# Performance work log

Hardware: AMD Instinct MI355X
Metric: run time of the kernel (lower is better)

The kernel has to match this reference:

```python
import jax, jax.numpy as jnp
import numpy as np

B, S, D, H, DH = 2, 2048, 768, 12, 64
GAMMA = 0.5
SMOOTHING = 1.0  # softmax_attn_smoothing scalar (non-trainable weight in the original)
SCALE = 1.0 / float(np.sqrt(DH))


def setup_inputs() -> dict:
    key = jax.random.key(0)
    ks = jax.random.split(key, 8)
    w = 0.02
    return {
        "inp": jax.random.normal(ks[0], (B, S, D), dtype=jnp.float32),
        "pos_emb": jax.random.normal(ks[1], (S, D), dtype=jnp.float32),
        "Wq_inp": jax.random.normal(ks[2], (D, H * DH), dtype=jnp.float32) * w,
        "Wk_inp": jax.random.normal(ks[3], (D, H * DH), dtype=jnp.float32) * w,
        "Wq_pos": jax.random.normal(ks[4], (D, H * DH), dtype=jnp.float32) * w,
        "Wk_pos": jax.random.normal(ks[5], (D, H * DH), dtype=jnp.float32) * w,
        "Wv": jax.random.normal(ks[6], (D, H * DH), dtype=jnp.float32) * w,
        "Wo": jax.random.normal(ks[7], (H * DH, D), dtype=jnp.float32) * w,
    }


def reference(inp, pos_emb, Wq_inp, Wk_inp, Wq_pos, Wk_pos, Wv, Wo):
    # projections; note original reshape order: [..., d_head, n_head]
    q_i = (inp @ Wq_inp).reshape(B, S, DH, H)
    k_i = (inp @ Wk_inp).reshape(B, S, DH, H)
    q_p = (pos_emb @ Wq_pos).reshape(S, DH, H)
    k_p = (pos_emb @ Wk_pos).reshape(S, DH, H)
    v = (inp @ Wv).reshape(B, S, DH, H)

    # content-content stream: [B,S,S,H], softmax over key axis (axis=2)
    score_inp = jnp.einsum("bidh,bjdh->bijh", q_i, k_i) * (SCALE * SMOOTHING)
    prob_inp = jax.nn.softmax(score_inp, axis=2)

    # position-position stream: [S,S,H], softmax over key axis (axis=1)
    score_pos = jnp.einsum("idh,jdh->ijh", q_p, k_p) * (SCALE * SMOOTHING)
    prob_pos = jax.nn.softmax(score_pos, axis=1)[None]  # [1,S,S,H]

    # gamma blend of the two attention distributions
    attn_prob = (1.0 - GAMMA) * prob_inp + GAMMA * prob_pos  # [B,S,S,H]

    # V-weighted sum, merge heads as [..., h, d] per the original 'bihd' output
    attn_out = jnp.einsum("bijh,bjdh->bihd", attn_prob, v).reshape(B, S, H * DH)
    attn_out = attn_out @ Wo  # [B,S,D]
    return attn_out, attn_prob
```

## Files before the change

kernel.cpp:

```cpp
#include <hip/hip_runtime.h>
#include <hip/hip_bf16.h>

constexpr int NH  = 12;
constexpr int SEQ = 2048;
constexpr int DHD = 64;
constexpr int DIM = 768;

typedef __bf16 bf16x8 __attribute__((ext_vector_type(8)));
typedef __bf16 bf16x4 __attribute__((ext_vector_type(4)));
typedef float  f32x4  __attribute__((ext_vector_type(4)));

#define MFMA16(a, b, c) __builtin_amdgcn_mfma_f32_16x16x32_bf16((a), (b), (c), 0, 0, 0)

__global__ __launch_bounds__(256) void proj_kernel(
    const float* __restrict__ inp, const float* __restrict__ pos,
    const float* __restrict__ Wqi, const float* __restrict__ Wki,
    const float* __restrict__ Wqp, const float* __restrict__ Wkp,
    const float* __restrict__ Wvv,
    __bf16* __restrict__ Qi, __bf16* __restrict__ Ki, __bf16* __restrict__ Vt,
    __bf16* __restrict__ Qp, __bf16* __restrict__ Kp)
{
    const int z = blockIdx.z;
    const float* A; const float* W; __bf16* outp; int M; int mode; float scale = 1.0f;
    if (z == 0)      { A = inp; W = Wqi; outp = Qi; M = 4096; mode = 0; scale = 0.125f; }
    else if (z == 1) { A = inp; W = Wki; outp = Ki; M = 4096; mode = 0; }
    else if (z == 2) { A = inp; W = Wvv; outp = Vt; M = 4096; mode = 1; }
    else if (z == 3) { A = pos; W = Wqp; outp = Qp; M = 2048; mode = 2; scale = 0.125f; }
    else             { A = pos; W = Wkp; outp = Kp; M = 2048; mode = 2; }

    const int m0 = blockIdx.y * 64;
    if (m0 >= M) return;
    const int n0 = blockIdx.x * 192;

    __shared__ __bf16 Al[64][32];
    __shared__ __bf16 Wl[192][32];

    const int tid = threadIdx.x;
    const int lane = tid & 63, wv = tid >> 6;
    const int wm = wv >> 1, wn = wv & 1;
    const int l15 = lane & 15, lg = lane >> 4;

    f32x4 c[2][6] = {};

    for (int kt = 0; kt < 24; ++kt) {
        const int k0 = kt * 32;
        __syncthreads();
        {
            const int r = tid >> 3, kq = tid & 7;
            #pragma unroll
            for (int rep = 0; rep < 2; ++rep) {
                const float4 v = *reinterpret_cast<const float4*>(
                    &A[(size_t)(m0 + r + rep * 32) * DIM + k0 + kq * 4]);
                bf16x4 t;
                t[0] = (__bf16)v.x; t[1] = (__bf16)v.y; t[2] = (__bf16)v.z; t[3] = (__bf16)v.w;
                *reinterpret_cast<bf16x4*>(&Al[r + rep * 32][kq * 4]) = t;
            }
        }
        for (int idx = tid; idx < 32 * 48; idx += 256) {
            const int k = idx / 48, nq = idx - k * 48;
            const float4 v = *reinterpret_cast<const float4*>(
                &W[(size_t)(k0 + k) * DIM + n0 + nq * 4]);
            Wl[nq * 4 + 0][k] = (__bf16)v.x;
            Wl[nq * 4 + 1][k] = (__bf16)v.y;
            Wl[nq * 4 + 2][k] = (__bf16)v.z;
            Wl[nq * 4 + 3][k] = (__bf16)v.w;
        }
        __syncthreads();

        bf16x8 a[2], b[6];
        #pragma unroll
        for (int mf = 0; mf < 2; ++mf)
            a[mf] = *reinterpret_cast<const bf16x8*>(&Al[wm * 32 + mf * 16 + l15][lg * 8]);
        #pragma unroll
        for (int nf = 0; nf < 6; ++nf)
            b[nf] = *reinterpret_cast<const bf16x8*>(&Wl[wn * 96 + nf * 16 + l15][lg * 8]);
        #pragma unroll
        for (int mf = 0; mf < 2; ++mf)
            #pragma unroll
            for (int nf = 0; nf < 6; ++nf)
                c[mf][nf] = MFMA16(a[mf], b[nf], c[mf][nf]);
    }

    #pragma unroll
    for (int mf = 0; mf < 2; ++mf)
        #pragma unroll
        for (int nf = 0; nf < 6; ++nf)
            #pragma unroll
            for (int r = 0; r < 4; ++r) {
                const int m = m0 + wm * 32 + mf * 16 + lg * 4 + r;
                const int n = n0 + wn * 96 + nf * 16 + l15;
                const float val = c[mf][nf][r] * scale;
                const int d = n / 12, hh = n - d * 12;
                size_t idx;
                if (mode == 0) {
                    const int b_ = m >> 11, s_ = m & 2047;
                    idx = (((size_t)b_ * NH + hh) * SEQ + s_) * DHD + d;
                } else if (mode == 1) {
                    const int b_ = m >> 11, s_ = m & 2047;
                    idx = (((size_t)b_ * NH + hh) * DHD + d) * SEQ + s_;
                } else {
                    idx = ((size_t)hh * SEQ + m) * DHD + d;
                }
                outp[idx] = (__bf16)val;
            }
}

__global__ __launch_bounds__(256) void stats_kernel(
    const __bf16* __restrict__ Qi, const __bf16* __restrict__ Ki,
    const __bf16* __restrict__ Qp, const __bf16* __restrict__ Kp,
    float* __restrict__ m_ws, float* __restrict__ l_ws)
{
    const int it = blockIdx.x, h = blockIdx.y, bb = blockIdx.z;
    const int tid = threadIdx.x, lane = tid & 63, wv = tid >> 6;
    const int l15 = lane & 15, lg = lane >> 4;
    const int i0 = it * 128 + wv * 32;

    const __bf16* Q = (bb < 2) ? Qi + ((size_t)bb * NH + h) * SEQ * DHD
                               : Qp + (size_t)h * SEQ * DHD;
    const __bf16* K = (bb < 2) ? Ki + ((size_t)bb * NH + h) * SEQ * DHD
                               : Kp + (size_t)h * SEQ * DHD;

    __shared__ __bf16 Klds[32][64];

    bf16x8 a[2][2];
    #pragma unroll
    for (int mf = 0; mf < 2; ++mf)
        #pragma unroll
        for (int ks = 0; ks < 2; ++ks)
            a[mf][ks] = *reinterpret_cast<const bf16x8*>(
                &Q[(size_t)(i0 + mf * 16 + l15) * DHD + ks * 32 + lg * 8]);

    float mr[2][4], lr[2][4];
    #pragma unroll
    for (int mf = 0; mf < 2; ++mf)
        #pragma unroll
        for (int r = 0; r < 4; ++r) { mr[mf][r] = -1e30f; lr[mf][r] = 0.0f; }

    for (int jt = 0; jt < 64; ++jt) {
        const int j0 = jt * 32;
        __syncthreads();
        {
            const int row = tid >> 3, kq = tid & 7;
            *reinterpret_cast<bf16x8*>(&Klds[row][kq * 8]) =
                *reinterpret_cast<const bf16x8*>(&K[(size_t)(j0 + row) * DHD + kq * 8]);
        }
        __syncthreads();

        f32x4 c[2][2] = {};
        #pragma unroll
        for (int ks = 0; ks < 2; ++ks) {
            const bf16x8 b0 = *reinterpret_cast<const bf16x8*>(&Klds[l15][ks * 32 + lg * 8]);
            const bf16x8 b1 = *reinterpret_cast<const bf16x8*>(&Klds[16 + l15][ks * 32 + lg * 8]);
            #pragma unroll
            for (int mf = 0; mf < 2; ++mf) {
                c[mf][0] = MFMA16(a[mf][ks], b0, c[mf][0]);
                c[mf][1] = MFMA16(a[mf][ks], b1, c[mf][1]);
            }
        }
        #pragma unroll
        for (int mf = 0; mf < 2; ++mf)
            #pragma unroll
            for (int r = 0; r < 4; ++r) {
                const float x0 = c[mf][0][r], x1 = c[mf][1][r];
                const float mn = fmaxf(mr[mf][r], fmaxf(x0, x1));
                lr[mf][r] = lr[mf][r] * __expf(mr[mf][r] - mn)
                          + __expf(x0 - mn) + __expf(x1 - mn);
                mr[mf][r] = mn;
            }
    }

    #pragma unroll
    for (int msk = 1; msk < 16; msk <<= 1)
        #pragma unroll
        for (int mf = 0; mf < 2; ++mf)
            #pragma unroll
            for (int r = 0; r < 4; ++r) {
                const float mo = __shfl_xor(mr[mf][r], msk);
                const float lo = __shfl_xor(lr[mf][r], msk);
                const float mn = fmaxf(mr[mf][r], mo);
                lr[mf][r] = lr[mf][r] * __expf(mr[mf][r] - mn) + lo * __expf(mo - mn);
                mr[mf][r] = mn;
            }

    if (l15 == 0) {
        const size_t base = ((size_t)bb * NH + h) * SEQ + i0;
        #pragma unroll
        for (int mf = 0; mf < 2; ++mf)
            #pragma unroll
            for (int r = 0; r < 4; ++r) {
                const int i = mf * 16 + lg * 4 + r;
                m_ws[base + i] = mr[mf][r];
                l_ws[base + i] = lr[mf][r];
            }
    }
}

__global__ __launch_bounds__(256) void emit_kernel(
    const __bf16* __restrict__ Qi, const __bf16* __restrict__ Ki,
    const __bf16* __restrict__ Qp, const __bf16* __restrict__ Kp,
    const __bf16* __restrict__ Vt,
    const float* __restrict__ m_ws, const float* __restrict__ l_ws,
    float* __restrict__ out1, float* __restrict__ attn_pre)
{
    const int it = blockIdx.x, js = blockIdx.y, b = blockIdx.z;
    const int i0 = it * 16;
    const int tid = threadIdx.x, lane = tid & 63, wv = tid >> 6;
    const int l15 = lane & 15, lg = lane >> 4;

    __shared__ __bf16 pbuf[12][16][32];
    __shared__ float  ml[12][16][4];

    if (tid < 192) {
        const int h = tid >> 4, i = tid & 15;
        const size_t bi  = ((size_t)b * NH + h) * SEQ + i0 + i;
        const size_t ppi = ((size_t)2 * NH + h) * SEQ + i0 + i;
        ml[h][i][0] = m_ws[bi];
        ml[h][i][1] = 1.0f / l_ws[bi];
        ml[h][i][2] = m_ws[ppi];
        ml[h][i][3] = 1.0f / l_ws[ppi];
    }
    __syncthreads();

    bf16x8 aQ[3][2][2];
    #pragma unroll
    for (int hh = 0; hh < 3; ++hh) {
        const int h = wv * 3 + hh;
        #pragma unroll
        for (int ks = 0; ks < 2; ++ks) {
            aQ[hh][0][ks] = *reinterpret_cast<const bf16x8*>(
                &Qi[(((size_t)b * NH + h) * SEQ + i0 + l15) * DHD + ks * 32 + lg * 8]);
            aQ[hh][1][ks] = *reinterpret_cast<const bf16x8*>(
                &Qp[((size_t)h * SEQ + i0 + l15) * DHD + ks * 32 + lg * 8]);
        }
    }

    f32x4 acc[3][4] = {};

    for (int jt = 0; jt < 16; ++jt) {
        const int j0 = js * 512 + jt * 32;

        #pragma unroll
        for (int hh = 0; hh < 3; ++hh) {
            const int h = wv * 3 + hh;
            const __bf16* Kib = Ki + ((size_t)b * NH + h) * SEQ * DHD;
            const __bf16* Kpb = Kp + (size_t)h * SEQ * DHD;

            f32x4 ci[2] = {}, cq[2] = {};
            #pragma unroll
            for (int ks = 0; ks < 2; ++ks)
                #pragma unroll
                for (int nf = 0; nf < 2; ++nf) {
                    const bf16x8 bi_ = *reinterpret_cast<const bf16x8*>(
                        &Kib[(size_t)(j0 + nf * 16 + l15) * DHD + ks * 32 + lg * 8]);
                    const bf16x8 bp_ = *reinterpret_cast<const bf16x8*>(
                        &Kpb[(size_t)(j0 + nf * 16 + l15) * DHD + ks * 32 + lg * 8]);
                    ci[nf] = MFMA16(aQ[hh][0][ks], bi_, ci[nf]);
                    cq[nf] = MFMA16(aQ[hh][1][ks], bp_, cq[nf]);
                }

            #pragma unroll
            for (int nf = 0; nf < 2; ++nf)
                #pragma unroll
                for (int r = 0; r < 4; ++r) {
                    const int i = lg * 4 + r;
                    const float pi_ = __expf(ci[nf][r] - ml[h][i][0]) * ml[h][i][1];
                    const float pq_ = __expf(cq[nf][r] - ml[h][i][2]) * ml[h][i][3];
                    pbuf[h][i][nf * 16 + l15] = (__bf16)(0.5f * pi_ + 0.5f * pq_);
                }

            const bf16x8 ap = *reinterpret_cast<const bf16x8*>(&pbuf[h][l15][lg * 8]);
            #pragma unroll
            for (int nf = 0; nf < 4; ++nf) {
                const bf16x8 bv = *reinterpret_cast<const bf16x8*>(
                    &Vt[(((size_t)b * NH + h) * DHD + nf * 16 + l15) * SEQ + j0 + lg * 8]);
                acc[hh][nf] = MFMA16(ap, bv, acc[hh][nf]);
            }
        }
        __syncthreads();

        #pragma unroll
        for (int rep = 0; rep < 2; ++rep) {
            const int pair = rep * 256 + tid;
            const int i = pair >> 5, jj = pair & 31;
            const size_t base = (((size_t)(b * SEQ + i0 + i)) * SEQ + j0 + jj) * 12;
            f32x4 v0, v1, v2;
            #pragma unroll
            for (int q = 0; q < 4; ++q) {
                v0[q] = (float)pbuf[q][i][jj];
                v1[q] = (float)pbuf[4 + q][i][jj];
                v2[q] = (float)pbuf[8 + q][i][jj];
            }
            *reinterpret_cast<f32x4*>(&out1[base])     = v0;
            *reinterpret_cast<f32x4*>(&out1[base + 4]) = v1;
            *reinterpret_cast<f32x4*>(&out1[base + 8]) = v2;
        }
        __syncthreads();
    }

    #pragma unroll
    for (int hh = 0; hh < 3; ++hh) {
        const int h = wv * 3 + hh;
        #pragma unroll
        for (int nf = 0; nf < 4; ++nf)
            #pragma unroll
            for (int r = 0; r < 4; ++r) {
                const int i = lg * 4 + r;
                atomicAdd(&attn_pre[((size_t)(b * SEQ + i0 + i)) * DIM + h * DHD + nf * 16 + l15],
                          acc[hh][nf][r]);
            }
    }
}

__global__ __launch_bounds__(256) void final_kernel(
    const float* __restrict__ A, const float* __restrict__ W, float* __restrict__ out0)
{
    const int m0 = blockIdx.y * 64;
    const int n0 = blockIdx.x * 192;

    __shared__ __bf16 Al[64][32];
    __shared__ __bf16 Wl[192][32];

    const int tid = threadIdx.x;
    const int lane = tid & 63, wv = tid >> 6;
    const int wm = wv >> 1, wn = wv & 1;
    const int l15 = lane & 15, lg = lane >> 4;

    f32x4 c[2][6] = {};

    for (int kt = 0; kt < 24; ++kt) {
        const int k0 = kt * 32;
        __syncthreads();
        {
            const int r = tid >> 3, kq = tid & 7;
            #pragma unroll
            for (int rep = 0; rep < 2; ++rep) {
                const float4 v = *reinterpret_cast<const float4*>(
                    &A[(size_t)(m0 + r + rep * 32) * DIM + k0 + kq * 4]);
                bf16x4 t;
                t[0] = (__bf16)v.x; t[1] = (__bf16)v.y; t[2] = (__bf16)v.z; t[3] = (__bf16)v.w;
                *reinterpret_cast<bf16x4*>(&Al[r + rep * 32][kq * 4]) = t;
            }
        }
        for (int idx = tid; idx < 32 * 48; idx += 256) {
            const int k = idx / 48, nq = idx - k * 48;
            const float4 v = *reinterpret_cast<const float4*>(
                &W[(size_t)(k0 + k) * DIM + n0 + nq * 4]);
            Wl[nq * 4 + 0][k] = (__bf16)v.x;
            Wl[nq * 4 + 1][k] = (__bf16)v.y;
            Wl[nq * 4 + 2][k] = (__bf16)v.z;
            Wl[nq * 4 + 3][k] = (__bf16)v.w;
        }
        __syncthreads();

        bf16x8 a[2], b[6];
        #pragma unroll
        for (int mf = 0; mf < 2; ++mf)
            a[mf] = *reinterpret_cast<const bf16x8*>(&Al[wm * 32 + mf * 16 + l15][lg * 8]);
        #pragma unroll
        for (int nf = 0; nf < 6; ++nf)
            b[nf] = *reinterpret_cast<const bf16x8*>(&Wl[wn * 96 + nf * 16 + l15][lg * 8]);
        #pragma unroll
        for (int mf = 0; mf < 2; ++mf)
            #pragma unroll
            for (int nf = 0; nf < 6; ++nf)
                c[mf][nf] = MFMA16(a[mf], b[nf], c[mf][nf]);
    }

    #pragma unroll
    for (int mf = 0; mf < 2; ++mf)
        #pragma unroll
        for (int nf = 0; nf < 6; ++nf)
            #pragma unroll
            for (int r = 0; r < 4; ++r) {
                const int m = m0 + wm * 32 + mf * 16 + lg * 4 + r;
                const int n = n0 + wn * 96 + nf * 16 + l15;
                out0[(size_t)m * DIM + n] = c[mf][nf][r];
            }
}

extern "C" void kernel_launch(void* const* d_in, const int* in_sizes, int n_in,
                              void* d_out, int out_size, void* d_ws, size_t ws_size,
                              hipStream_t stream)
{
    (void)in_sizes; (void)n_in; (void)out_size; (void)ws_size;

    const float* inp = (const float*)d_in[0];
    const float* pos = (const float*)d_in[1];
    const float* Wqi = (const float*)d_in[2];
    const float* Wki = (const float*)d_in[3];
    const float* Wqp = (const float*)d_in[4];
    const float* Wkp = (const float*)d_in[5];
    const float* Wvv = (const float*)d_in[6];
    const float* Wo  = (const float*)d_in[7];

    char* w = (char*)d_ws;
    __bf16* Qi = (__bf16*)w; w += (size_t)2 * NH * SEQ * DHD * 2;
    __bf16* Ki = (__bf16*)w; w += (size_t)2 * NH * SEQ * DHD * 2;
    __bf16* Vt = (__bf16*)w; w += (size_t)2 * NH * SEQ * DHD * 2;
    __bf16* Qp = (__bf16*)w; w += (size_t)NH * SEQ * DHD * 2;
    __bf16* Kp = (__bf16*)w; w += (size_t)NH * SEQ * DHD * 2;
    float* m_ws = (float*)w; w += (size_t)3 * NH * SEQ * 4;
    float* l_ws = (float*)w; w += (size_t)3 * NH * SEQ * 4;
    float* attn_pre = (float*)w; w += (size_t)4096 * DIM * 4;

    float* out0 = (float*)d_out;
    float* out1 = out0 + (size_t)2 * SEQ * DIM;

    hipMemsetAsync(attn_pre, 0, (size_t)4096 * DIM * 4, stream);

    hipLaunchKernelGGL(proj_kernel, dim3(4, 64, 5), dim3(256), 0, stream,
                       inp, pos, Wqi, Wki, Wqp, Wkp, Wvv, Qi, Ki, Vt, Qp, Kp);
    hipLaunchKernelGGL(stats_kernel, dim3(16, 12, 3), dim3(256), 0, stream,
                       Qi, Ki, Qp, Kp, m_ws, l_ws);
    hipLaunchKernelGGL(emit_kernel, dim3(128, 4, 2), dim3(256), 0, stream,
                       Qi, Ki, Qp, Kp, Vt, m_ws, l_ws, out1, attn_pre);
    hipLaunchKernelGGL(final_kernel, dim3(4, 64, 1), dim3(256), 0, stream,
                       attn_pre, Wo, out0);
}
```

Baseline: 848.6 us.

## Stage projection outputs through LDS, shrink stats tiles, per-wave emit buffers

The projection kernel now transposes its output tile through shared memory so Q/K/V stores go out as 16-byte vectors instead of scattered 2-byte writes. The stats kernel drops its LDS K tile and block barriers: each wave loads K fragments straight from global memory into registers over 16-row tiles, and the grid doubles. The emit kernel gives each wave private P buffers, removing block-wide syncs around the attention-probability writeout. It also folds the 0.5 blend weight into the normalizers, halves the key span per block and doubles the grid. The trade-off is narrower per-lane scalar stores to out1 and more atomic adds into attn_pre from the larger emit grid.

```diff
diff --git a/kernel.cpp b/kernel.cpp
--- a/kernel.cpp
+++ b/kernel.cpp
@@ -32,8 +32,10 @@
     if (m0 >= M) return;
     const int n0 = blockIdx.x * 192;
 
-    __shared__ __bf16 Al[64][32];
-    __shared__ __bf16 Wl[192][32];
+    __shared__ __align__(16) char smraw[27648];
+    auto Al = reinterpret_cast<__bf16(*)[32]>(smraw);
+    auto Wl = reinterpret_cast<__bf16(*)[32]>(smraw + 4096);
+    auto oT = reinterpret_cast<__bf16(*)[72]>(smraw);
 
     const int tid = threadIdx.x;
     const int lane = tid & 63, wv = tid >> 6;
@@ -81,28 +83,51 @@
                 c[mf][nf] = MFMA16(a[mf], b[nf], c[mf][nf]);
     }
 
+    __syncthreads();
     #pragma unroll
     for (int mf = 0; mf < 2; ++mf)
         #pragma unroll
-        for (int nf = 0; nf < 6; ++nf)
-            #pragma unroll
-            for (int r = 0; r < 4; ++r) {
-                const int m = m0 + wm * 32 + mf * 16 + lg * 4 + r;
-                const int n = n0 + wn * 96 + nf * 16 + l15;
-                const float val = c[mf][nf][r] * scale;
-                const int d = n / 12, hh = n - d * 12;
-                size_t idx;
-                if (mode == 0) {
-                    const int b_ = m >> 11, s_ = m & 2047;
-                    idx = (((size_t)b_ * NH + hh) * SEQ + s_) * DHD + d;
-                } else if (mode == 1) {
-                    const int b_ = m >> 11, s_ = m & 2047;
-                    idx = (((size_t)b_ * NH + hh) * DHD + d) * SEQ + s_;
-                } else {
-                    idx = ((size_t)hh * SEQ + m) * DHD + d;
-                }
-                outp[idx] = (__bf16)val;
-            }
+        for (int nf = 0; nf < 6; ++nf) {
+            bf16x4 t;
+            #pragma unroll
+            for (int r = 0; r < 4; ++r) t[r] = (__bf16)(c[mf][nf][r] * scale);
+            *reinterpret_cast<bf16x4*>(&oT[wn * 96 + nf * 16 + l15][wm * 32 + mf * 16 + lg * 4]) = t;
+        }
+    __syncthreads();
+
+    if (mode == 1) {
+        if (tid < 192) {
+            const int nl = tid;
+            const int h = nl % 12, d = (n0 / 12) + nl / 12;
+            const int b_ = m0 >> 11, s0 = m0 & 2047;
+            const size_t base = (((size_t)b_ * NH + h) * DHD + d) * SEQ + s0;
+            #pragma unroll
+            for (int q = 0; q < 8; ++q)
+                *reinterpret_cast<bf16x8*>(&outp[base + q * 8]) =
+                    *reinterpret_cast<const bf16x8*>(&oT[nl][q * 8]);
+        }
+    } else {
+        const int d0 = n0 / 12;
+        #pragma unroll
+        for (int rep = 0; rep < 3; ++rep) {
+            const int cc = rep * 256 + tid;
+            const int s = cc / 12, h = cc - s * 12;
+            size_t base;
+            if (mode == 0) {
+                const int b_ = m0 >> 11, sg = (m0 & 2047) + s;
+                base = (((size_t)b_ * NH + h) * SEQ + sg) * DHD + d0;
+            } else {
+                base = ((size_t)h * SEQ + m0 + s) * DHD + d0;
+            }
+            bf16x8 v0, v1;
+            #pragma unroll
+            for (int d = 0; d < 8; ++d) v0[d] = oT[d * 12 + h][s];
+            #pragma unroll
+            for (int d = 0; d < 8; ++d) v1[d] = oT[(8 + d) * 12 + h][s];
+            *reinterpret_cast<bf16x8*>(&outp[base])     = v0;
+            *reinterpret_cast<bf16x8*>(&outp[base + 8]) = v1;
+        }
+    }
 }
 
 __global__ __launch_bounds__(256) void stats_kernel(
@@ -113,85 +138,69 @@
     const int it = blockIdx.x, h = blockIdx.y, bb = blockIdx.z;
     const int tid = threadIdx.x, lane = tid & 63, wv = tid >> 6;
     const int l15 = lane & 15, lg = lane >> 4;
-    const int i0 = it * 128 + wv * 32;
+    const int i0 = it * 64 + wv * 16;
 
     const __bf16* Q = (bb < 2) ? Qi + ((size_t)bb * NH + h) * SEQ * DHD
                                : Qp + (size_t)h * SEQ * DHD;
     const __bf16* K = (bb < 2) ? Ki + ((size_t)bb * NH + h) * SEQ * DHD
                                : Kp + (size_t)h * SEQ * DHD;
 
-    __shared__ __bf16 Klds[32][64];
-
-    bf16x8 a[2][2];
-    #pragma unroll
-    for (int mf = 0; mf < 2; ++mf)
+    bf16x8 a[2];
+    #pragma unroll
+    for (int ks = 0; ks < 2; ++ks)
+        a[ks] = *reinterpret_cast<const bf16x8*>(
+            &Q[(size_t)(i0 + l15) * DHD + ks * 32 + lg * 8]);
+
+    float mr[4], lr[4];
+    #pragma unroll
+    for (int r = 0; r < 4; ++r) { mr[r] = -1e30f; lr[r] = 0.0f; }
+
+    for (int jt = 0; jt < 32; ++jt) {
+        const int j0 = jt * 64;
+        bf16x8 bk[2][4];
         #pragma unroll
         for (int ks = 0; ks < 2; ++ks)
-            a[mf][ks] = *reinterpret_cast<const bf16x8*>(
-                &Q[(size_t)(i0 + mf * 16 + l15) * DHD + ks * 32 + lg * 8]);
-
-    float mr[2][4], lr[2][4];
-    #pragma unroll
-    for (int mf = 0; mf < 2; ++mf)
-        #pragma unroll
-        for (int r = 0; r < 4; ++r) { mr[mf][r] = -1e30f; lr[mf][r] = 0.0f; }
-
-    for (int jt = 0; jt < 64; ++jt) {
-        const int j0 = jt * 32;
-        __syncthreads();
-        {
-            const int row = tid >> 3, kq = tid & 7;
-            *reinterpret_cast<bf16x8*>(&Klds[row][kq * 8]) =
-                *reinterpret_cast<const bf16x8*>(&K[(size_t)(j0 + row) * DHD + kq * 8]);
-        }
-        __syncthreads();
-
-        f32x4 c[2][2] = {};
-        #pragma unroll
-        for (int ks = 0; ks < 2; ++ks) {
-            const bf16x8 b0 = *reinterpret_cast<const bf16x8*>(&Klds[l15][ks * 32 + lg * 8]);
-            const bf16x8 b1 = *reinterpret_cast<const bf16x8*>(&Klds[16 + l15][ks * 32 + lg * 8]);
-            #pragma unroll
-            for (int mf = 0; mf < 2; ++mf) {
-                c[mf][0] = MFMA16(a[mf][ks], b0, c[mf][0]);
-                c[mf][1] = MFMA16(a[mf][ks], b1, c[mf][1]);
-            }
-        }
-        #pragma unroll
-        for (int mf = 0; mf < 2; ++mf)
-            #pragma unroll
-            for (int r = 0; r < 4; ++r) {
-                const float x0 = c[mf][0][r], x1 = c[mf][1][r];
-                const float mn = fmaxf(mr[mf][r], fmaxf(x0, x1));
-                lr[mf][r] = lr[mf][r] * __expf(mr[mf][r] - mn)
-                          + __expf(x0 - mn) + __expf(x1 - mn);
-                mr[mf][r] = mn;
-            }
+            #pragma unroll
+            for (int nf = 0; nf < 4; ++nf)
+                bk[ks][nf] = *reinterpret_cast<const bf16x8*>(
+                    &K[(size_t)(j0 + nf * 16 + l15) * DHD + ks * 32 + lg * 8]);
+        f32x4 c[4] = {};
+        #pragma unroll
+        for (int ks = 0; ks < 2; ++ks)
+            #pragma unroll
+            for (int nf = 0; nf < 4; ++nf)
+                c[nf] = MFMA16(a[ks], bk[ks][nf], c[nf]);
+
+        #pragma unroll
+        for (int r = 0; r < 4; ++r) {
+            const float x01 = fmaxf(c[0][r], c[1][r]);
+            const float x23 = fmaxf(c[2][r], c[3][r]);
+            const float mn = fmaxf(mr[r], fmaxf(x01, x23));
+            lr[r] = lr[r] * __expf(mr[r] - mn)
+                  + __expf(c[0][r] - mn) + __expf(c[1][r] - mn)
+                  + __expf(c[2][r] - mn) + __expf(c[3][r] - mn);
+            mr[r] = mn;
+        }
     }
 
     #pragma unroll
     for (int msk = 1; msk < 16; msk <<= 1)
         #pragma unroll
-        for (int mf = 0; mf < 2; ++mf)
-            #pragma unroll
-            for (int r = 0; r < 4; ++r) {
-                const float mo = __shfl_xor(mr[mf][r], msk);
-                const float lo = __shfl_xor(lr[mf][r], msk);
-                const float mn = fmaxf(mr[mf][r], mo);
-                lr[mf][r] = lr[mf][r] * __expf(mr[mf][r] - mn) + lo * __expf(mo - mn);
-                mr[mf][r] = mn;
-            }
+        for (int r = 0; r < 4; ++r) {
+            const float mo = __shfl_xor(mr[r], msk);
+            const float lo = __shfl_xor(lr[r], msk);
+            const float mn = fmaxf(mr[r], mo);
+            lr[r] = lr[r] * __expf(mr[r] - mn) + lo * __expf(mo - mn);
+            mr[r] = mn;
+        }
 
     if (l15 == 0) {
         const size_t base = ((size_t)bb * NH + h) * SEQ + i0;
         #pragma unroll
-        for (int mf = 0; mf < 2; ++mf)
-            #pragma unroll
-            for (int r = 0; r < 4; ++r) {
-                const int i = mf * 16 + lg * 4 + r;
-                m_ws[base + i] = mr[mf][r];
-                l_ws[base + i] = lr[mf][r];
-            }
+        for (int r = 0; r < 4; ++r) {
+            m_ws[base + lg * 4 + r] = mr[r];
+            l_ws[base + lg * 4 + r] = lr[r];
+        }
     }
 }
 
@@ -207,17 +216,18 @@
     const int tid = threadIdx.x, lane = tid & 63, wv = tid >> 6;
     const int l15 = lane & 15, lg = lane >> 4;
 
-    __shared__ __bf16 pbuf[12][16][32];
-    __shared__ float  ml[12][16][4];
-
-    if (tid < 192) {
-        const int h = tid >> 4, i = tid & 15;
+    __shared__ __bf16 pbuf[4][3][16][40];
+    __shared__ float  mlb[4][3][16][4];
+
+    if (lane < 48) {
+        const int hh = lane >> 4, i = lane & 15;
+        const int h = wv * 3 + hh;
         const size_t bi  = ((size_t)b * NH + h) * SEQ + i0 + i;
         const size_t ppi = ((size_t)2 * NH + h) * SEQ + i0 + i;
-        ml[h][i][0] = m_ws[bi];
-        ml[h][i][1] = 1.0f / l_ws[bi];
-        ml[h][i][2] = m_ws[ppi];
-        ml[h][i][3] = 1.0f / l_ws[ppi];
+        mlb[wv][hh][i][0] = m_ws[bi];
+        mlb[wv][hh][i][1] = 0.5f / l_ws[bi];
+        mlb[wv][hh][i][2] = m_ws[ppi];
+        mlb[wv][hh][i][3] = 0.5f / l_ws[ppi];
     }
     __syncthreads();
 
@@ -236,8 +246,9 @@
 
     f32x4 acc[3][4] = {};
 
-    for (int jt = 0; jt < 16; ++jt) {
-        const int j0 = js * 512 + jt * 32;
+    #pragma unroll 1
+    for (int jt = 0; jt < 8; ++jt) {
+        const int j0 = js * 256 + jt * 32;
 
         #pragma unroll
         for (int hh = 0; hh < 3; ++hh) {
@@ -259,16 +270,18 @@
                 }
 
             #pragma unroll
-            for (int nf = 0; nf < 2; ++nf)
+            for (int r = 0; r < 4; ++r) {
+                const int i = lg * 4 + r;
+                const f32x4 mlv = *reinterpret_cast<const f32x4*>(&mlb[wv][hh][i][0]);
                 #pragma unroll
-                for (int r = 0; r < 4; ++r) {
-                    const int i = lg * 4 + r;
-                    const float pi_ = __expf(ci[nf][r] - ml[h][i][0]) * ml[h][i][1];
-                    const float pq_ = __expf(cq[nf][r] - ml[h][i][2]) * ml[h][i][3];
-                    pbuf[h][i][nf * 16 + l15] = (__bf16)(0.5f * pi_ + 0.5f * pq_);
+                for (int nf = 0; nf < 2; ++nf) {
+                    const float pi_ = __expf(ci[nf][r] - mlv[0]) * mlv[1];
+                    const float pq_ = __expf(cq[nf][r] - mlv[2]) * mlv[3];
+                    pbuf[wv][hh][i][nf * 16 + l15] = (__bf16)(pi_ + pq_);
                 }
-
-            const bf16x8 ap = *reinterpret_cast<const bf16x8*>(&pbuf[h][l15][lg * 8]);
+            }
+
+            const bf16x8 ap = *reinterpret_cast<const bf16x8*>(&pbuf[wv][hh][l15][lg * 8]);
             #pragma unroll
             for (int nf = 0; nf < 4; ++nf) {
                 const bf16x8 bv = *reinterpret_cast<const bf16x8*>(
@@ -276,25 +289,17 @@
                 acc[hh][nf] = MFMA16(ap, bv, acc[hh][nf]);
             }
         }
-        __syncthreads();
-
-        #pragma unroll
-        for (int rep = 0; rep < 2; ++rep) {
-            const int pair = rep * 256 + tid;
+
+        #pragma unroll
+        for (int p = 0; p < 8; ++p) {
+            const int pair = p * 64 + lane;
             const int i = pair >> 5, jj = pair & 31;
-            const size_t base = (((size_t)(b * SEQ + i0 + i)) * SEQ + j0 + jj) * 12;
-            f32x4 v0, v1, v2;
-            #pragma unroll
-            for (int q = 0; q < 4; ++q) {
-                v0[q] = (float)pbuf[q][i][jj];
-                v1[q] = (float)pbuf[4 + q][i][jj];
-                v2[q] = (float)pbuf[8 + q][i][jj];
-            }
-            *reinterpret_cast<f32x4*>(&out1[base])     = v0;
-            *reinterpret_cast<f32x4*>(&out1[base + 4]) = v1;
-            *reinterpret_cast<f32x4*>(&out1[base + 8]) = v2;
-        }
-        __syncthreads();
+            const size_t base =
+                (((size_t)(b * SEQ + i0 + i)) * SEQ + j0 + jj) * 12 + wv * 3;
+            out1[base + 0] = (float)pbuf[wv][0][i][jj];
+            out1[base + 1] = (float)pbuf[wv][1][i][jj];
+            out1[base + 2] = (float)pbuf[wv][2][i][jj];
+        }
     }
 
     #pragma unroll
@@ -410,9 +415,9 @@
 
     hipLaunchKernelGGL(proj_kernel, dim3(4, 64, 5), dim3(256), 0, stream,
                        inp, pos, Wqi, Wki, Wqp, Wkp, Wvv, Qi, Ki, Vt, Qp, Kp);
-    hipLaunchKernelGGL(stats_kernel, dim3(16, 12, 3), dim3(256), 0, stream,
+    hipLaunchKernelGGL(stats_kernel, dim3(32, 12, 3), dim3(256), 0, stream,
                        Qi, Ki, Qp, Kp, m_ws, l_ws);
-    hipLaunchKernelGGL(emit_kernel, dim3(128, 4, 2), dim3(256), 0, stream,
+    hipLaunchKernelGGL(emit_kernel, dim3(128, 8, 2), dim3(256), 0, stream,
                        Qi, Ki, Qp, Kp, Vt, m_ws, l_ws, out1, attn_pre);
     hipLaunchKernelGGL(final_kernel, dim3(4, 64, 1), dim3(256), 0, stream,
                        attn_pre, Wo, out0);
```

New measurement: 995.9 us. 17.4% more time.

## Use exp2 with folded log2e, single-wave stats, double-buffered emit with nontemporal stores

Applied to the files above, without the earlier changes.

Several changes are bundled. The log2(e) factor is folded into the Q scale so softmax can use exp2f, and the 0.5 gamma factor is folded into the inverse normalisers. The stats kernel becomes one wave per block that loads K straight from global memory with 64-wide key tiles, dropping LDS and barriers. The emit kernel double-buffers pbuf with padded rows, removes one barrier per tile, splits the key range across twice as many blocks, and writes the large attention-probability output with nontemporal stores. The extra key splits mean more atomicAdd traffic into attn_pre.

```diff
diff --git a/kernel.cpp b/kernel.cpp
--- a/kernel.cpp
+++ b/kernel.cpp
@@ -5,6 +5,7 @@
 constexpr int SEQ = 2048;
 constexpr int DHD = 64;
 constexpr int DIM = 768;
+constexpr float QSCALE = 0.125f * 1.44269504088896f;
 
 typedef __bf16 bf16x8 __attribute__((ext_vector_type(8)));
 typedef __bf16 bf16x4 __attribute__((ext_vector_type(4)));
@@ -22,10 +23,10 @@
 {
     const int z = blockIdx.z;
     const float* A; const float* W; __bf16* outp; int M; int mode; float scale = 1.0f;
-    if (z == 0)      { A = inp; W = Wqi; outp = Qi; M = 4096; mode = 0; scale = 0.125f; }
+    if (z == 0)      { A = inp; W = Wqi; outp = Qi; M = 4096; mode = 0; scale = QSCALE; }
     else if (z == 1) { A = inp; W = Wki; outp = Ki; M = 4096; mode = 0; }
     else if (z == 2) { A = inp; W = Wvv; outp = Vt; M = 4096; mode = 1; }
-    else if (z == 3) { A = pos; W = Wqp; outp = Qp; M = 2048; mode = 2; scale = 0.125f; }
+    else if (z == 3) { A = pos; W = Wqp; outp = Qp; M = 2048; mode = 2; scale = QSCALE; }
     else             { A = pos; W = Wkp; outp = Kp; M = 2048; mode = 2; }
 
     const int m0 = blockIdx.y * 64;
@@ -105,23 +106,21 @@
             }
 }
 
-__global__ __launch_bounds__(256) void stats_kernel(
+__global__ __launch_bounds__(64) void stats_kernel(
     const __bf16* __restrict__ Qi, const __bf16* __restrict__ Ki,
     const __bf16* __restrict__ Qp, const __bf16* __restrict__ Kp,
     float* __restrict__ m_ws, float* __restrict__ l_ws)
 {
-    const int it = blockIdx.x, h = blockIdx.y, bb = blockIdx.z;
-    const int tid = threadIdx.x, lane = tid & 63, wv = tid >> 6;
+    const int bx = blockIdx.x, h = blockIdx.y, bb = blockIdx.z;
+    const int lane = threadIdx.x;
     const int l15 = lane & 15, lg = lane >> 4;
-    const int i0 = it * 128 + wv * 32;
+    const int i0 = bx * 32;
 
     const __bf16* Q = (bb < 2) ? Qi + ((size_t)bb * NH + h) * SEQ * DHD
                                : Qp + (size_t)h * SEQ * DHD;
     const __bf16* K = (bb < 2) ? Ki + ((size_t)bb * NH + h) * SEQ * DHD
                                : Kp + (size_t)h * SEQ * DHD;
 
-    __shared__ __bf16 Klds[32][64];
-
     bf16x8 a[2][2];
     #pragma unroll
     for (int mf = 0; mf < 2; ++mf)
@@ -136,35 +135,34 @@
         #pragma unroll
         for (int r = 0; r < 4; ++r) { mr[mf][r] = -1e30f; lr[mf][r] = 0.0f; }
 
-    for (int jt = 0; jt < 64; ++jt) {
-        const int j0 = jt * 32;
-        __syncthreads();
-        {
-            const int row = tid >> 3, kq = tid & 7;
-            *reinterpret_cast<bf16x8*>(&Klds[row][kq * 8]) =
-                *reinterpret_cast<const bf16x8*>(&K[(size_t)(j0 + row) * DHD + kq * 8]);
-        }
-        __syncthreads();
-
-        f32x4 c[2][2] = {};
-        #pragma unroll
-        for (int ks = 0; ks < 2; ++ks) {
-            const bf16x8 b0 = *reinterpret_cast<const bf16x8*>(&Klds[l15][ks * 32 + lg * 8]);
-            const bf16x8 b1 = *reinterpret_cast<const bf16x8*>(&Klds[16 + l15][ks * 32 + lg * 8]);
-            #pragma unroll
-            for (int mf = 0; mf < 2; ++mf) {
-                c[mf][0] = MFMA16(a[mf][ks], b0, c[mf][0]);
-                c[mf][1] = MFMA16(a[mf][ks], b1, c[mf][1]);
-            }
-        }
-        #pragma unroll
-        for (int mf = 0; mf < 2; ++mf)
-            #pragma unroll
-            for (int r = 0; r < 4; ++r) {
-                const float x0 = c[mf][0][r], x1 = c[mf][1][r];
-                const float mn = fmaxf(mr[mf][r], fmaxf(x0, x1));
-                lr[mf][r] = lr[mf][r] * __expf(mr[mf][r] - mn)
-                          + __expf(x0 - mn) + __expf(x1 - mn);
+    for (int jt = 0; jt < 32; ++jt) {
+        const int j0 = jt * 64;
+        bf16x8 bk[2][4];
+        #pragma unroll
+        for (int ks = 0; ks < 2; ++ks)
+            #pragma unroll
+            for (int nf = 0; nf < 4; ++nf)
+                bk[ks][nf] = *reinterpret_cast<const bf16x8*>(
+                    &K[(size_t)(j0 + nf * 16 + l15) * DHD + ks * 32 + lg * 8]);
+        f32x4 c[2][4] = {};
+        #pragma unroll
+        for (int ks = 0; ks < 2; ++ks)
+            #pragma unroll
+            for (int nf = 0; nf < 4; ++nf)
+                #pragma unroll
+                for (int mf = 0; mf < 2; ++mf)
+                    c[mf][nf] = MFMA16(a[mf][ks], bk[ks][nf], c[mf][nf]);
+
+        #pragma unroll
+        for (int mf = 0; mf < 2; ++mf)
+            #pragma unroll
+            for (int r = 0; r < 4; ++r) {
+                const float x01 = fmaxf(c[mf][0][r], c[mf][1][r]);
+                const float x23 = fmaxf(c[mf][2][r], c[mf][3][r]);
+                const float mn = fmaxf(mr[mf][r], fmaxf(x01, x23));
+                lr[mf][r] = lr[mf][r] * exp2f(mr[mf][r] - mn)
+                          + exp2f(c[mf][0][r] - mn) + exp2f(c[mf][1][r] - mn)
+                          + exp2f(c[mf][2][r] - mn) + exp2f(c[mf][3][r] - mn);
                 mr[mf][r] = mn;
             }
     }
@@ -178,7 +176,7 @@
                 const float mo = __shfl_xor(mr[mf][r], msk);
                 const float lo = __shfl_xor(lr[mf][r], msk);
                 const float mn = fmaxf(mr[mf][r], mo);
-                lr[mf][r] = lr[mf][r] * __expf(mr[mf][r] - mn) + lo * __expf(mo - mn);
+                lr[mf][r] = lr[mf][r] * exp2f(mr[mf][r] - mn) + lo * exp2f(mo - mn);
                 mr[mf][r] = mn;
             }
 
@@ -188,9 +186,8 @@
         for (int mf = 0; mf < 2; ++mf)
             #pragma unroll
             for (int r = 0; r < 4; ++r) {
-                const int i = mf * 16 + lg * 4 + r;
-                m_ws[base + i] = mr[mf][r];
-                l_ws[base + i] = lr[mf][r];
+                m_ws[base + mf * 16 + lg * 4 + r] = mr[mf][r];
+                l_ws[base + mf * 16 + lg * 4 + r] = lr[mf][r];
             }
     }
 }
@@ -207,17 +204,17 @@
     const int tid = threadIdx.x, lane = tid & 63, wv = tid >> 6;
     const int l15 = lane & 15, lg = lane >> 4;
 
-    __shared__ __bf16 pbuf[12][16][32];
-    __shared__ float  ml[12][16][4];
+    __shared__ __align__(16) __bf16 pbuf[2][12][16][40];
+    __shared__ float ml[12][16][4];
 
     if (tid < 192) {
         const int h = tid >> 4, i = tid & 15;
         const size_t bi  = ((size_t)b * NH + h) * SEQ + i0 + i;
         const size_t ppi = ((size_t)2 * NH + h) * SEQ + i0 + i;
         ml[h][i][0] = m_ws[bi];
-        ml[h][i][1] = 1.0f / l_ws[bi];
+        ml[h][i][1] = 0.5f / l_ws[bi];
         ml[h][i][2] = m_ws[ppi];
-        ml[h][i][3] = 1.0f / l_ws[ppi];
+        ml[h][i][3] = 0.5f / l_ws[ppi];
     }
     __syncthreads();
 
@@ -236,8 +233,10 @@
 
     f32x4 acc[3][4] = {};
 
-    for (int jt = 0; jt < 16; ++jt) {
-        const int j0 = js * 512 + jt * 32;
+    #pragma unroll 1
+    for (int jt = 0; jt < 8; ++jt) {
+        const int j0 = js * 256 + jt * 32;
+        const int buf = jt & 1;
 
         #pragma unroll
         for (int hh = 0; hh < 3; ++hh) {
@@ -259,16 +258,18 @@
                 }
 
             #pragma unroll
-            for (int nf = 0; nf < 2; ++nf)
+            for (int r = 0; r < 4; ++r) {
+                const int i = lg * 4 + r;
+                const f32x4 mlv = *reinterpret_cast<const f32x4*>(&ml[h][i][0]);
                 #pragma unroll
-                for (int r = 0; r < 4; ++r) {
-                    const int i = lg * 4 + r;
-                    const float pi_ = __expf(ci[nf][r] - ml[h][i][0]) * ml[h][i][1];
-                    const float pq_ = __expf(cq[nf][r] - ml[h][i][2]) * ml[h][i][3];
-                    pbuf[h][i][nf * 16 + l15] = (__bf16)(0.5f * pi_ + 0.5f * pq_);
+                for (int nf = 0; nf < 2; ++nf) {
+                    const float pi_ = exp2f(ci[nf][r] - mlv[0]) * mlv[1];
+                    const float pq_ = exp2f(cq[nf][r] - mlv[2]) * mlv[3];
+                    pbuf[buf][h][i][nf * 16 + l15] = (__bf16)(pi_ + pq_);
                 }
-
-            const bf16x8 ap = *reinterpret_cast<const bf16x8*>(&pbuf[h][l15][lg * 8]);
+            }
+
+            const bf16x8 ap = *reinterpret_cast<const bf16x8*>(&pbuf[buf][h][l15][lg * 8]);
             #pragma unroll
             for (int nf = 0; nf < 4; ++nf) {
                 const bf16x8 bv = *reinterpret_cast<const bf16x8*>(
@@ -286,15 +287,14 @@
             f32x4 v0, v1, v2;
             #pragma unroll
             for (int q = 0; q < 4; ++q) {
-                v0[q] = (float)pbuf[q][i][jj];
-                v1[q] = (float)pbuf[4 + q][i][jj];
-                v2[q] = (float)pbuf[8 + q][i][jj];
-            }
-            *reinterpret_cast<f32x4*>(&out1[base])     = v0;
-            *reinterpret_cast<f32x4*>(&out1[base + 4]) = v1;
-            *reinterpret_cast<f32x4*>(&out1[base + 8]) = v2;
-        }
-        __syncthreads();
+                v0[q] = (float)pbuf[buf][q][i][jj];
+                v1[q] = (float)pbuf[buf][4 + q][i][jj];
+                v2[q] = (float)pbuf[buf][8 + q][i][jj];
+            }
+            __builtin_nontemporal_store(v0, reinterpret_cast<f32x4*>(&out1[base]));
+            __builtin_nontemporal_store(v1, reinterpret_cast<f32x4*>(&out1[base + 4]));
+            __builtin_nontemporal_store(v2, reinterpret_cast<f32x4*>(&out1[base + 8]));
+        }
     }
 
     #pragma unroll
@@ -410,9 +410,9 @@
 
     hipLaunchKernelGGL(proj_kernel, dim3(4, 64, 5), dim3(256), 0, stream,
                        inp, pos, Wqi, Wki, Wqp, Wkp, Wvv, Qi, Ki, Vt, Qp, Kp);
-    hipLaunchKernelGGL(stats_kernel, dim3(16, 12, 3), dim3(256), 0, stream,
+    hipLaunchKernelGGL(stats_kernel, dim3(64, 12, 3), dim3(64), 0, stream,
                        Qi, Ki, Qp, Kp, m_ws, l_ws);
-    hipLaunchKernelGGL(emit_kernel, dim3(128, 4, 2), dim3(256), 0, stream,
+    hipLaunchKernelGGL(emit_kernel, dim3(128, 8, 2), dim3(256), 0, stream,
                        Qi, Ki, Qp, Kp, Vt, m_ws, l_ws, out1, attn_pre);
     hipLaunchKernelGGL(final_kernel, dim3(4, 64, 1), dim3(256), 0, stream,
                        attn_pre, Wo, out0);
```

New measurement: 891.5 us. 5.1% more time.
